# Optimization experiments

Measured on AMD Instinct MI355X. Metric: run time of the kernel, lower is better.

Reference implementation:

```python
import jax, jax.numpy as jnp
import numpy as np

N_PARENTS = 4096   # parent clusters
K = 32             # points decoded per cluster
NEIGH = 128        # neigh_dec_size
FEAT = 256         # input_size (per-parent feature dim passed through)


def setup_inputs() -> dict:
    key = jax.random.key(0)
    ks = jax.random.split(key, 6)
    def lin(k, fan_in, fan_out):
        return jax.random.normal(k, (fan_in, fan_out), jnp.float32) / np.sqrt(fan_in).astype(np.float32)
    return {
        "input_features": jax.random.normal(ks[0], (N_PARENTS, NEIGH + FEAT), jnp.float32),
        # neighborhood decoder: Linear NEIGH -> K*3 (relative points)
        "W_dec": lin(ks[1], NEIGH, K * 3), "b_dec": jnp.zeros((K * 3,), jnp.float32),
        # fc chain: (FEAT+3) -> 512 -> 512 -> 256
        "W1": lin(ks[2], FEAT + 3, 512), "b1": jnp.zeros((512,), jnp.float32),
        "W2": lin(ks[3], 512, 512),      "b2": jnp.zeros((512,), jnp.float32),
        "W3": lin(ks[4], 512, 256),      "b3": jnp.zeros((256,), jnp.float32),
    }


def reference(input_features, W_dec, b_dec, W1, b1, W2, b2, W3, b3):
    # split: first NEIGH dims go to the neighborhood decoder, rest are parent features
    neigh_feats = input_features[:, :NEIGH]            # [N, NEIGH]
    features = input_features[:, NEIGH:]               # [N, FEAT]

    # neighborhood_dec: decode K relative 3D points per parent + cluster assignment
    relative_points = (neigh_feats @ W_dec + b_dec).reshape(-1, 3)   # [N*K, 3]
    cluster = jnp.repeat(jnp.arange(N_PARENTS, dtype=jnp.int32), K)  # [N*K]

    # gather parent features per point, concat with relative points
    features_dup = features[cluster]                                  # [N*K, FEAT]
    h = jnp.concatenate([features_dup, relative_points], axis=1)      # [N*K, FEAT+3]

    # chained Linear + ReLU (leaky=False)
    h = jax.nn.relu(h @ W1 + b1)
    h = jax.nn.relu(h @ W2 + b2)
    h = jax.nn.relu(h @ W3 + b3)
    return relative_points, h, cluster
```

## Files before the change

kernel.cpp:

```cpp
#include <hip/hip_runtime.h>
#include <hip/hip_bf16.h>

typedef unsigned short u16;
typedef unsigned int   u32;

#define NP     4096
#define NCH    131072
#define HBASE  393216
#define CLBASE 33947648

#define WS_W2F   0
#define WS_W3F   524288
#define WS_W1AF  786432
#define WS_F1    1048576

using bf16x8 = __attribute__((ext_vector_type(8))) short;
using f32x4  = __attribute__((ext_vector_type(4))) float;

__device__ inline u16 f2bf(float x) {
  union { float f; u32 u; } v; v.f = x;
  u32 r = v.u + 0x7FFFu + ((v.u >> 16) & 1u);
  return (u16)(r >> 16);
}
__device__ inline u32 pack2(float a, float b) {
  return (u32)f2bf(a) | ((u32)f2bf(b) << 16);
}

__global__ __launch_bounds__(256) void k_prep(const float* __restrict__ W1,
                                              const float* __restrict__ W2,
                                              const float* __restrict__ W3,
                                              u16* __restrict__ w1af,
                                              u16* __restrict__ w2f,
                                              u16* __restrict__ w3f,
                                              float* __restrict__ out) {
  int b = blockIdx.x, t = threadIdx.x;
  if (b >= 512) {
    int idx = (b - 512) * 256 + t;
    out[CLBASE + idx] = (float)(idx >> 5);
    return;
  }
  __shared__ float tile[32][33];
  const float* src; u16* dst; int pitchN, kt, nt, nkc;
  if (b < 128)      { src = W1; dst = w1af; pitchN = 512; kt = b & 7;  nt = b >> 3; nkc = 8;  }
  else if (b < 384) { int bb = b - 128; src = W2; dst = w2f; pitchN = 512; kt = bb & 15; nt = bb >> 4; nkc = 16; }
  else              { int bb = b - 384; src = W3; dst = w3f; pitchN = 256; kt = bb & 15; nt = bb >> 4; nkc = 16; }
  {
    int kk = t >> 3, n4 = (t & 7) * 4;
    const float4 v = *(const float4*)(src + (kt * 32 + kk) * pitchN + nt * 32 + n4);
    tile[kk][n4 + 0] = v.x; tile[kk][n4 + 1] = v.y;
    tile[kk][n4 + 2] = v.z; tile[kk][n4 + 3] = v.w;
  }
  __syncthreads();
  {
    int s = t >> 1, half = t & 1, fr = s >> 6, l = s & 63;
    int n_l = fr * 16 + (l & 15);
    int k_l = (l >> 4) * 8 + half * 4;
    uint2 o;
    o.x = pack2(tile[k_l + 0][n_l], tile[k_l + 1][n_l]);
    o.y = pack2(tile[k_l + 2][n_l], tile[k_l + 3][n_l]);
    int frag_id = (nt * 2 + fr) * nkc + kt;
    *(uint2*)(dst + frag_id * 512 + l * 8 + half * 4) = o;
  }
}

__global__ __launch_bounds__(512) void k_rel(const float* __restrict__ in_feats,
                                             const float* __restrict__ Wd,
                                             const float* __restrict__ bd,
                                             float* __restrict__ out) {
  int p0 = blockIdx.x * 4, t = threadIdx.x;
  __shared__ float wd[12288];
  __shared__ float ne[512];
  __shared__ float bds[96];
#pragma unroll
  for (int i = 0; i < 6; ++i)
    *(float4*)(wd + (i * 512 + t) * 4) = *(const float4*)(Wd + (i * 512 + t) * 4);
  { int pp = t >> 7, k = t & 127; ne[t] = in_feats[(p0 + pp) * 384 + k]; }
  if (t < 96) bds[t] = bd[t];
  __syncthreads();
  if (t < 384) {
    int pp = t / 96, c = t - pp * 96;
    float acc = bds[c];
    const float* nep = ne + pp * 128;
#pragma unroll 4
    for (int k = 0; k < 128; ++k) acc += nep[k] * wd[k * 96 + c];
    out[(p0 + pp) * 96 + c] = acc;
  }
}

__global__ __launch_bounds__(512, 2) void k_f1(const float* __restrict__ in_feats,
                                               const float* __restrict__ b1,
                                               const u16* __restrict__ w1af,
                                               float* __restrict__ F1) {
  int p0 = blockIdx.x * 16;
  int tid = threadIdx.x, lane = tid & 63, w = tid >> 6;
  __shared__ u16 sh_a[16 * 256];
  __shared__ float b1s[512];
  b1s[tid] = b1[tid];
  {
    int r = tid >> 5, k0 = (tid & 31) * 8;
    const float4 v0 = *(const float4*)(in_feats + (p0 + r) * 384 + 128 + k0);
    const float4 v1 = *(const float4*)(in_feats + (p0 + r) * 384 + 128 + k0 + 4);
    uint4 o;
    o.x = pack2(v0.x, v0.y); o.y = pack2(v0.z, v0.w);
    o.z = pack2(v1.x, v1.y); o.w = pack2(v1.z, v1.w);
    int slot = (k0 >> 3) ^ (r & 7);
    *(uint4*)(sh_a + r * 256 + slot * 8) = o;
  }
  __syncthreads();
  f32x4 acc[4];
#pragma unroll
  for (int i = 0; i < 4; ++i) acc[i] = f32x4{0.f, 0.f, 0.f, 0.f};
  int col = lane & 15, q8 = (lane >> 4) * 8;
#pragma unroll
  for (int kc = 0; kc < 8; ++kc) {
    int slot = ((kc * 32 + q8) >> 3) ^ (col & 7);
    bf16x8 a = *(const bf16x8*)(sh_a + col * 256 + slot * 8);
#pragma unroll
    for (int nf = 0; nf < 4; ++nf) {
      bf16x8 bfr = *(const bf16x8*)(w1af + ((w * 4 + nf) * 8 + kc) * 512 + lane * 8);
      acc[nf] = __builtin_amdgcn_mfma_f32_16x16x32_bf16(a, bfr, acc[nf], 0, 0, 0);
    }
  }
  int rb = (lane >> 4) * 4;
#pragma unroll
  for (int nf = 0; nf < 4; ++nf) {
    int n = w * 64 + nf * 16 + col;
#pragma unroll
    for (int i = 0; i < 4; ++i)
      F1[(p0 + rb + i) * 512 + n] = acc[nf][i] + b1s[n];
  }
}

__global__ __launch_bounds__(512, 2) void k_main(const float* __restrict__ W1,
                                                 const float* __restrict__ b2,
                                                 const float* __restrict__ b3,
                                                 const u16* __restrict__ w2f,
                                                 const u16* __restrict__ w3f,
                                                 const float* __restrict__ F1,
                                                 float* __restrict__ out) {
  int blk = blockIdx.x;
  int tid = threadIdx.x, lane = tid & 63, w = tid >> 6;
  __shared__ u16 sh_h[128 * 512];
  __shared__ float f1s[2048], w1bs[1536], b2s[512], b3s[256], rels[384];

  *(float4*)(f1s + tid * 4) = *(const float4*)(F1 + blk * 2048 + tid * 4);
  w1bs[tid]        = W1[131072 + tid];
  w1bs[tid + 512]  = W1[131072 + 512 + tid];
  w1bs[tid + 1024] = W1[131072 + 1024 + tid];
  b2s[tid] = b2[tid];
  if (tid < 256) b3s[tid] = b3[tid];
  if (tid < 384) rels[tid] = out[blk * 384 + tid];
  __syncthreads();

  {
    int rbase = tid & 31, g = tid >> 5;
#pragma unroll
    for (int rr = 0; rr < 128; rr += 32) {
      int r = rr + rbase, pp = r >> 5;
      float r0 = rels[r * 3 + 0], r1 = rels[r * 3 + 1], r2 = rels[r * 3 + 2];
#pragma unroll
      for (int gg = 0; gg < 8; ++gg) {
        int c4 = g * 4 + gg * 64;
        const float4 f  = *(const float4*)(f1s + pp * 512 + c4);
        const float4 w0 = *(const float4*)(w1bs + c4);
        const float4 w1v = *(const float4*)(w1bs + 512 + c4);
        const float4 w2v = *(const float4*)(w1bs + 1024 + c4);
        float v0 = fmaxf(f.x + r0 * w0.x + r1 * w1v.x + r2 * w2v.x, 0.f);
        float v1 = fmaxf(f.y + r0 * w0.y + r1 * w1v.y + r2 * w2v.y, 0.f);
        float v2 = fmaxf(f.z + r0 * w0.z + r1 * w1v.z + r2 * w2v.z, 0.f);
        float v3 = fmaxf(f.w + r0 * w0.w + r1 * w1v.w + r2 * w2v.w, 0.f);
        uint2 o; o.x = pack2(v0, v1); o.y = pack2(v2, v3);
        int slot = (c4 >> 3) ^ (r & 7);
        *(uint2*)(sh_h + r * 512 + slot * 8 + (g & 1) * 4) = o;
      }
    }
  }
  __syncthreads();

  int col = lane & 15, q8 = (lane >> 4) * 8;

  f32x4 acc2[8][4];
#pragma unroll
  for (int mf = 0; mf < 8; ++mf)
#pragma unroll
    for (int nf = 0; nf < 4; ++nf) acc2[mf][nf] = f32x4{0.f, 0.f, 0.f, 0.f};
#pragma unroll 2
  for (int kc = 0; kc < 16; ++kc) {
    bf16x8 bfr[4];
#pragma unroll
    for (int nf = 0; nf < 4; ++nf)
      bfr[nf] = *(const bf16x8*)(w2f + ((w * 4 + nf) * 16 + kc) * 512 + lane * 8);
#pragma unroll
    for (int mf = 0; mf < 8; ++mf) {
      int row = mf * 16 + col;
      int slot = ((kc * 32 + q8) >> 3) ^ (row & 7);
      bf16x8 a = *(const bf16x8*)(sh_h + row * 512 + slot * 8);
#pragma unroll
      for (int nf = 0; nf < 4; ++nf)
        acc2[mf][nf] = __builtin_amdgcn_mfma_f32_16x16x32_bf16(a, bfr[nf], acc2[mf][nf], 0, 0, 0);
    }
  }
  __syncthreads();

  {
    int rq = (lane >> 4) * 4;
#pragma unroll
    for (int mf = 0; mf < 8; ++mf)
#pragma unroll
      for (int nf = 0; nf < 4; ++nf) {
        int n = w * 64 + nf * 16 + col;
#pragma unroll
        for (int i = 0; i < 4; ++i) {
          int r = mf * 16 + rq + i;
          float v = fmaxf(acc2[mf][nf][i] + b2s[n], 0.f);
          sh_h[r * 512 + (((n >> 3) ^ (r & 7)) << 3) + (n & 7)] = f2bf(v);
        }
      }
  }
  __syncthreads();

  f32x4 acc3[8][2];
#pragma unroll
  for (int mf = 0; mf < 8; ++mf)
#pragma unroll
    for (int nf = 0; nf < 2; ++nf) acc3[mf][nf] = f32x4{0.f, 0.f, 0.f, 0.f};
#pragma unroll 2
  for (int kc = 0; kc < 16; ++kc) {
    bf16x8 bfr[2];
#pragma unroll
    for (int nf = 0; nf < 2; ++nf)
      bfr[nf] = *(const bf16x8*)(w3f + ((w * 2 + nf) * 16 + kc) * 512 + lane * 8);
#pragma unroll
    for (int mf = 0; mf < 8; ++mf) {
      int row = mf * 16 + col;
      int slot = ((kc * 32 + q8) >> 3) ^ (row & 7);
      bf16x8 a = *(const bf16x8*)(sh_h + row * 512 + slot * 8);
#pragma unroll
      for (int nf = 0; nf < 2; ++nf)
        acc3[mf][nf] = __builtin_amdgcn_mfma_f32_16x16x32_bf16(a, bfr[nf], acc3[mf][nf], 0, 0, 0);
    }
  }

  {
    int rq = (lane >> 4) * 4;
#pragma unroll
    for (int mf = 0; mf < 8; ++mf)
#pragma unroll
      for (int nf = 0; nf < 2; ++nf) {
        int n = w * 32 + nf * 16 + col;
#pragma unroll
        for (int i = 0; i < 4; ++i) {
          int r = mf * 16 + rq + i;
          float v = fmaxf(acc3[mf][nf][i] + b3s[n], 0.f);
          out[HBASE + (blk * 128 + r) * 256 + n] = v;
        }
      }
  }
}

extern "C" void kernel_launch(void* const* d_in, const int* in_sizes, int n_in,
                              void* d_out, int out_size, void* d_ws, size_t ws_size,
                              hipStream_t stream) {
  const float* in_feats = (const float*)d_in[0];
  const float* Wd = (const float*)d_in[1];
  const float* bd = (const float*)d_in[2];
  const float* W1 = (const float*)d_in[3];
  const float* b1 = (const float*)d_in[4];
  const float* W2 = (const float*)d_in[5];
  const float* b2 = (const float*)d_in[6];
  const float* W3 = (const float*)d_in[7];
  const float* b3 = (const float*)d_in[8];
  float* out = (float*)d_out;
  char* ws = (char*)d_ws;
  u16*   w2f  = (u16*)(ws + WS_W2F);
  u16*   w3f  = (u16*)(ws + WS_W3F);
  u16*   w1af = (u16*)(ws + WS_W1AF);
  float* F1   = (float*)(ws + WS_F1);

  k_prep<<<1024, 256, 0, stream>>>(W1, W2, W3, w1af, w2f, w3f, out);
  k_rel<<<1024, 512, 0, stream>>>(in_feats, Wd, bd, out);
  k_f1<<<256, 512, 0, stream>>>(in_feats, b1, w1af, F1);
  k_main<<<1024, 512, 0, stream>>>(W1, b2, b3, w2f, w3f, F1, out);
}
```

Baseline: 272.6 us.

## Merge prep kernels into one launch and double-buffer weight fragments in main GEMMs

Folds the weight-prep, relative-point decoder, first-layer feature GEMM and cluster-index fill into a single multi-role kernel, dropping three launches to one. W1 is now read directly from fp32 and packed to bf16 inside the F1 GEMM instead of through a pre-swizzled buffer. In the main kernel the W2/W3 B-fragments are double-buffered across k-steps, the LDS swizzle gains extra row bits, the layer-1 build writes 16-byte chunks, and outputs use nontemporal stores. Risks include uncoalesced strided W1 reads in the F1 path and higher register pressure from double buffering.

```diff
diff --git a/kernel.cpp b/kernel.cpp
--- a/kernel.cpp
+++ b/kernel.cpp
@@ -11,123 +11,128 @@
 
 #define WS_W2F   0
 #define WS_W3F   524288
-#define WS_W1AF  786432
 #define WS_F1    1048576
 
 using bf16x8 = __attribute__((ext_vector_type(8))) short;
 using f32x4  = __attribute__((ext_vector_type(4))) float;
 
-__device__ inline u16 f2bf(float x) {
-  union { float f; u32 u; } v; v.f = x;
-  u32 r = v.u + 0x7FFFu + ((v.u >> 16) & 1u);
-  return (u16)(r >> 16);
-}
-__device__ inline u32 pack2(float a, float b) {
-  return (u32)f2bf(a) | ((u32)f2bf(b) << 16);
-}
-
-__global__ __launch_bounds__(256) void k_prep(const float* __restrict__ W1,
-                                              const float* __restrict__ W2,
-                                              const float* __restrict__ W3,
-                                              u16* __restrict__ w1af,
-                                              u16* __restrict__ w2f,
-                                              u16* __restrict__ w3f,
-                                              float* __restrict__ out) {
-  int b = blockIdx.x, t = threadIdx.x;
-  if (b >= 512) {
-    int idx = (b - 512) * 256 + t;
-    out[CLBASE + idx] = (float)(idx >> 5);
-    return;
-  }
-  __shared__ float tile[32][33];
-  const float* src; u16* dst; int pitchN, kt, nt, nkc;
-  if (b < 128)      { src = W1; dst = w1af; pitchN = 512; kt = b & 7;  nt = b >> 3; nkc = 8;  }
-  else if (b < 384) { int bb = b - 128; src = W2; dst = w2f; pitchN = 512; kt = bb & 15; nt = bb >> 4; nkc = 16; }
-  else              { int bb = b - 384; src = W3; dst = w3f; pitchN = 256; kt = bb & 15; nt = bb >> 4; nkc = 16; }
-  {
-    int kk = t >> 3, n4 = (t & 7) * 4;
-    const float4 v = *(const float4*)(src + (kt * 32 + kk) * pitchN + nt * 32 + n4);
-    tile[kk][n4 + 0] = v.x; tile[kk][n4 + 1] = v.y;
-    tile[kk][n4 + 2] = v.z; tile[kk][n4 + 3] = v.w;
-  }
-  __syncthreads();
-  {
-    int s = t >> 1, half = t & 1, fr = s >> 6, l = s & 63;
-    int n_l = fr * 16 + (l & 15);
-    int k_l = (l >> 4) * 8 + half * 4;
-    uint2 o;
-    o.x = pack2(tile[k_l + 0][n_l], tile[k_l + 1][n_l]);
-    o.y = pack2(tile[k_l + 2][n_l], tile[k_l + 3][n_l]);
-    int frag_id = (nt * 2 + fr) * nkc + kt;
-    *(uint2*)(dst + frag_id * 512 + l * 8 + half * 4) = o;
-  }
-}
-
-__global__ __launch_bounds__(512) void k_rel(const float* __restrict__ in_feats,
-                                             const float* __restrict__ Wd,
-                                             const float* __restrict__ bd,
-                                             float* __restrict__ out) {
-  int p0 = blockIdx.x * 4, t = threadIdx.x;
-  __shared__ float wd[12288];
-  __shared__ float ne[512];
-  __shared__ float bds[96];
-#pragma unroll
-  for (int i = 0; i < 6; ++i)
-    *(float4*)(wd + (i * 512 + t) * 4) = *(const float4*)(Wd + (i * 512 + t) * 4);
-  { int pp = t >> 7, k = t & 127; ne[t] = in_feats[(p0 + pp) * 384 + k]; }
-  if (t < 96) bds[t] = bd[t];
-  __syncthreads();
-  if (t < 384) {
-    int pp = t / 96, c = t - pp * 96;
-    float acc = bds[c];
-    const float* nep = ne + pp * 128;
+__device__ inline u32 pk2(float a, float b) {
+  __hip_bfloat162 h = __float22bfloat162_rn(make_float2(a, b));
+  return *reinterpret_cast<u32*>(&h);
+}
+
+__device__ inline int swz(int r, int cg) {
+  return cg ^ (r & 7) ^ ((r >> 3) & 3);
+}
+
+__global__ __launch_bounds__(512, 2) void k_pre(const float* __restrict__ in_feats,
+                                                const float* __restrict__ Wd,
+                                                const float* __restrict__ bd,
+                                                const float* __restrict__ W1,
+                                                const float* __restrict__ b1,
+                                                const float* __restrict__ W2,
+                                                const float* __restrict__ W3,
+                                                u16* __restrict__ w2f,
+                                                u16* __restrict__ w3f,
+                                                float* __restrict__ F1,
+                                                float* __restrict__ out) {
+  __shared__ __align__(16) char smem[51584];
+  int b = blockIdx.x, tid = threadIdx.x;
+
+  if (b < 256) {
+    u16*   sh_a = (u16*)smem;
+    float* b1s  = (float*)(smem + 8192);
+    int p0 = b * 16, lane = tid & 63, w = tid >> 6;
+    b1s[tid] = b1[tid];
+    {
+      int r = tid >> 5, k0 = (tid & 31) * 8;
+      const float4 v0 = *(const float4*)(in_feats + (p0 + r) * 384 + 128 + k0);
+      const float4 v1 = *(const float4*)(in_feats + (p0 + r) * 384 + 128 + k0 + 4);
+      uint4 o;
+      o.x = pk2(v0.x, v0.y); o.y = pk2(v0.z, v0.w);
+      o.z = pk2(v1.x, v1.y); o.w = pk2(v1.z, v1.w);
+      int slot = (k0 >> 3) ^ (r & 7);
+      *(uint4*)(sh_a + r * 256 + slot * 8) = o;
+    }
+    __syncthreads();
+    f32x4 acc[4];
+#pragma unroll
+    for (int i = 0; i < 4; ++i) acc[i] = f32x4{0.f, 0.f, 0.f, 0.f};
+    int col = lane & 15, q = lane >> 4, q8 = q * 8;
+#pragma unroll
+    for (int kc = 0; kc < 8; ++kc) {
+      int slot = ((kc * 32 + q8) >> 3) ^ (col & 7);
+      bf16x8 a = *(const bf16x8*)(sh_a + col * 256 + slot * 8);
+#pragma unroll
+      for (int nf = 0; nf < 4; ++nf) {
+        const float* wp = W1 + (kc * 32 + q8) * 512 + (w * 4 + nf) * 16 + col;
+        float v0 = wp[0],      v1 = wp[512],  v2 = wp[1024], v3 = wp[1536];
+        float v4 = wp[2048],   v5 = wp[2560], v6 = wp[3072], v7 = wp[3584];
+        union { bf16x8 v; u32 u[4]; } uu;
+        uu.u[0] = pk2(v0, v1); uu.u[1] = pk2(v2, v3);
+        uu.u[2] = pk2(v4, v5); uu.u[3] = pk2(v6, v7);
+        acc[nf] = __builtin_amdgcn_mfma_f32_16x16x32_bf16(a, uu.v, acc[nf], 0, 0, 0);
+      }
+    }
+    int rb = (lane >> 4) * 4;
+#pragma unroll
+    for (int nf = 0; nf < 4; ++nf) {
+      int n = w * 64 + nf * 16 + col;
+#pragma unroll
+      for (int i = 0; i < 4; ++i)
+        F1[(p0 + rb + i) * 512 + n] = acc[nf][i] + b1s[n];
+    }
+  } else if (b < 1280) {
+    float* wd  = (float*)smem;
+    float* ne  = (float*)(smem + 49152);
+    float* bds = (float*)(smem + 51200);
+    int p0 = (b - 256) * 4, t = tid;
+#pragma unroll
+    for (int i = 0; i < 6; ++i)
+      *(float4*)(wd + (i * 512 + t) * 4) = *(const float4*)(Wd + (i * 512 + t) * 4);
+    { int pp = t >> 7, k = t & 127; ne[t] = in_feats[(p0 + pp) * 384 + k]; }
+    if (t < 96) bds[t] = bd[t];
+    __syncthreads();
+    if (t < 384) {
+      int pp = t / 96, c = t - pp * 96;
+      float acc = bds[c];
+      const float* nep = ne + pp * 128;
 #pragma unroll 4
-    for (int k = 0; k < 128; ++k) acc += nep[k] * wd[k * 96 + c];
-    out[(p0 + pp) * 96 + c] = acc;
-  }
-}
-
-__global__ __launch_bounds__(512, 2) void k_f1(const float* __restrict__ in_feats,
-                                               const float* __restrict__ b1,
-                                               const u16* __restrict__ w1af,
-                                               float* __restrict__ F1) {
-  int p0 = blockIdx.x * 16;
-  int tid = threadIdx.x, lane = tid & 63, w = tid >> 6;
-  __shared__ u16 sh_a[16 * 256];
-  __shared__ float b1s[512];
-  b1s[tid] = b1[tid];
-  {
-    int r = tid >> 5, k0 = (tid & 31) * 8;
-    const float4 v0 = *(const float4*)(in_feats + (p0 + r) * 384 + 128 + k0);
-    const float4 v1 = *(const float4*)(in_feats + (p0 + r) * 384 + 128 + k0 + 4);
-    uint4 o;
-    o.x = pack2(v0.x, v0.y); o.y = pack2(v0.z, v0.w);
-    o.z = pack2(v1.x, v1.y); o.w = pack2(v1.z, v1.w);
-    int slot = (k0 >> 3) ^ (r & 7);
-    *(uint4*)(sh_a + r * 256 + slot * 8) = o;
-  }
-  __syncthreads();
-  f32x4 acc[4];
-#pragma unroll
-  for (int i = 0; i < 4; ++i) acc[i] = f32x4{0.f, 0.f, 0.f, 0.f};
-  int col = lane & 15, q8 = (lane >> 4) * 8;
-#pragma unroll
-  for (int kc = 0; kc < 8; ++kc) {
-    int slot = ((kc * 32 + q8) >> 3) ^ (col & 7);
-    bf16x8 a = *(const bf16x8*)(sh_a + col * 256 + slot * 8);
-#pragma unroll
-    for (int nf = 0; nf < 4; ++nf) {
-      bf16x8 bfr = *(const bf16x8*)(w1af + ((w * 4 + nf) * 8 + kc) * 512 + lane * 8);
-      acc[nf] = __builtin_amdgcn_mfma_f32_16x16x32_bf16(a, bfr, acc[nf], 0, 0, 0);
-    }
-  }
-  int rb = (lane >> 4) * 4;
-#pragma unroll
-  for (int nf = 0; nf < 4; ++nf) {
-    int n = w * 64 + nf * 16 + col;
-#pragma unroll
-    for (int i = 0; i < 4; ++i)
-      F1[(p0 + rb + i) * 512 + n] = acc[nf][i] + b1s[n];
+      for (int k = 0; k < 128; ++k) acc += nep[k] * wd[k * 96 + c];
+      out[(p0 + pp) * 96 + c] = acc;
+    }
+  } else if (b < 1472) {
+    float (*tile)[32][33] = (float (*)[32][33])smem;
+    int h = tid >> 8, t = tid & 255;
+    const float* src; u16* dst; int pitchN, g;
+    if (b < 1408) { g = (b - 1280) * 2 + h; src = W2; dst = w2f; pitchN = 512; }
+    else          { g = (b - 1408) * 2 + h; src = W3; dst = w3f; pitchN = 256; }
+    int kt = g & 15, nt = g >> 4;
+    {
+      int kk = t >> 3, n4 = (t & 7) * 4;
+      const float4 v = *(const float4*)(src + (kt * 32 + kk) * pitchN + nt * 32 + n4);
+      tile[h][kk][n4 + 0] = v.x; tile[h][kk][n4 + 1] = v.y;
+      tile[h][kk][n4 + 2] = v.z; tile[h][kk][n4 + 3] = v.w;
+    }
+    __syncthreads();
+    {
+      int s = t >> 1, half = t & 1, fr = s >> 6, l = s & 63;
+      int n_l = fr * 16 + (l & 15);
+      int k_l = (l >> 4) * 8 + half * 4;
+      uint2 o;
+      o.x = pk2(tile[h][k_l + 0][n_l], tile[h][k_l + 1][n_l]);
+      o.y = pk2(tile[h][k_l + 2][n_l], tile[h][k_l + 3][n_l]);
+      int frag_id = (nt * 2 + fr) * 16 + kt;
+      *(uint2*)(dst + frag_id * 512 + l * 8 + half * 4) = o;
+    }
+  } else {
+    int idx = ((b - 1472) * 512 + tid) * 4;
+    float c = (float)(idx >> 5);
+    float* p = out + CLBASE + idx;
+    __builtin_nontemporal_store(c, p + 0);
+    __builtin_nontemporal_store(c, p + 1);
+    __builtin_nontemporal_store(c, p + 2);
+    __builtin_nontemporal_store(c, p + 3);
   }
 }
 
@@ -153,25 +158,34 @@
   __syncthreads();
 
   {
-    int rbase = tid & 31, g = tid >> 5;
+    int r = tid & 31, g = tid >> 5;
 #pragma unroll
     for (int rr = 0; rr < 128; rr += 32) {
-      int r = rr + rbase, pp = r >> 5;
-      float r0 = rels[r * 3 + 0], r1 = rels[r * 3 + 1], r2 = rels[r * 3 + 2];
-#pragma unroll
-      for (int gg = 0; gg < 8; ++gg) {
-        int c4 = g * 4 + gg * 64;
-        const float4 f  = *(const float4*)(f1s + pp * 512 + c4);
-        const float4 w0 = *(const float4*)(w1bs + c4);
-        const float4 w1v = *(const float4*)(w1bs + 512 + c4);
-        const float4 w2v = *(const float4*)(w1bs + 1024 + c4);
-        float v0 = fmaxf(f.x + r0 * w0.x + r1 * w1v.x + r2 * w2v.x, 0.f);
-        float v1 = fmaxf(f.y + r0 * w0.y + r1 * w1v.y + r2 * w2v.y, 0.f);
-        float v2 = fmaxf(f.z + r0 * w0.z + r1 * w1v.z + r2 * w2v.z, 0.f);
-        float v3 = fmaxf(f.w + r0 * w0.w + r1 * w1v.w + r2 * w2v.w, 0.f);
-        uint2 o; o.x = pack2(v0, v1); o.y = pack2(v2, v3);
-        int slot = (c4 >> 3) ^ (r & 7);
-        *(uint2*)(sh_h + r * 512 + slot * 8 + (g & 1) * 4) = o;
+      int row = rr + r, pp = rr >> 5;
+      float r0 = rels[row * 3 + 0], r1 = rels[row * 3 + 1], r2 = rels[row * 3 + 2];
+#pragma unroll
+      for (int gg = 0; gg < 4; ++gg) {
+        int c8 = g * 8 + gg * 128;
+        const float4 fa = *(const float4*)(f1s + pp * 512 + c8);
+        const float4 fb = *(const float4*)(f1s + pp * 512 + c8 + 4);
+        const float4 wa0 = *(const float4*)(w1bs + c8);
+        const float4 wb0 = *(const float4*)(w1bs + c8 + 4);
+        const float4 wa1 = *(const float4*)(w1bs + 512 + c8);
+        const float4 wb1 = *(const float4*)(w1bs + 512 + c8 + 4);
+        const float4 wa2 = *(const float4*)(w1bs + 1024 + c8);
+        const float4 wb2 = *(const float4*)(w1bs + 1024 + c8 + 4);
+        float v0 = fmaxf(fa.x + r0 * wa0.x + r1 * wa1.x + r2 * wa2.x, 0.f);
+        float v1 = fmaxf(fa.y + r0 * wa0.y + r1 * wa1.y + r2 * wa2.y, 0.f);
+        float v2 = fmaxf(fa.z + r0 * wa0.z + r1 * wa1.z + r2 * wa2.z, 0.f);
+        float v3 = fmaxf(fa.w + r0 * wa0.w + r1 * wa1.w + r2 * wa2.w, 0.f);
+        float v4 = fmaxf(fb.x + r0 * wb0.x + r1 * wb1.x + r2 * wb2.x, 0.f);
+        float v5 = fmaxf(fb.y + r0 * wb0.y + r1 * wb1.y + r2 * wb2.y, 0.f);
+        float v6 = fmaxf(fb.z + r0 * wb0.z + r1 * wb1.z + r2 * wb2.z, 0.f);
+        float v7 = fmaxf(fb.w + r0 * wb0.w + r1 * wb1.w + r2 * wb2.w, 0.f);
+        uint4 o;
+        o.x = pk2(v0, v1); o.y = pk2(v2, v3);
+        o.z = pk2(v4, v5); o.w = pk2(v6, v7);
+        *(uint4*)(sh_h + row * 512 + swz(row, c8 >> 3) * 8) = o;
       }
     }
   }
@@ -184,20 +198,29 @@
   for (int mf = 0; mf < 8; ++mf)
 #pragma unroll
     for (int nf = 0; nf < 4; ++nf) acc2[mf][nf] = f32x4{0.f, 0.f, 0.f, 0.f};
+  {
+    const u16* w2p = w2f + (size_t)(w * 4 * 16) * 512 + lane * 8;
+    bf16x8 bufA[4], bufB[4];
+#pragma unroll
+    for (int nf = 0; nf < 4; ++nf) bufA[nf] = *(const bf16x8*)(w2p + nf * 16 * 512);
 #pragma unroll 2
-  for (int kc = 0; kc < 16; ++kc) {
-    bf16x8 bfr[4];
-#pragma unroll
-    for (int nf = 0; nf < 4; ++nf)
-      bfr[nf] = *(const bf16x8*)(w2f + ((w * 4 + nf) * 16 + kc) * 512 + lane * 8);
-#pragma unroll
-    for (int mf = 0; mf < 8; ++mf) {
-      int row = mf * 16 + col;
-      int slot = ((kc * 32 + q8) >> 3) ^ (row & 7);
-      bf16x8 a = *(const bf16x8*)(sh_h + row * 512 + slot * 8);
-#pragma unroll
-      for (int nf = 0; nf < 4; ++nf)
-        acc2[mf][nf] = __builtin_amdgcn_mfma_f32_16x16x32_bf16(a, bfr[nf], acc2[mf][nf], 0, 0, 0);
+    for (int kc = 0; kc < 16; ++kc) {
+      const bf16x8* cur = (kc & 1) ? bufB : bufA;
+      bf16x8* nxt = (kc & 1) ? bufA : bufB;
+      if (kc < 15) {
+#pragma unroll
+        for (int nf = 0; nf < 4; ++nf)
+          nxt[nf] = *(const bf16x8*)(w2p + (nf * 16 + kc + 1) * 512);
+      }
+      int cb = (kc * 32 + q8) >> 3;
+#pragma unroll
+      for (int mf = 0; mf < 8; ++mf) {
+        int row = mf * 16 + col;
+        bf16x8 a = *(const bf16x8*)(sh_h + row * 512 + swz(row, cb) * 8);
+#pragma unroll
+        for (int nf = 0; nf < 4; ++nf)
+          acc2[mf][nf] = __builtin_amdgcn_mfma_f32_16x16x32_bf16(a, cur[nf], acc2[mf][nf], 0, 0, 0);
+      }
     }
   }
   __syncthreads();
@@ -208,51 +231,64 @@
     for (int mf = 0; mf < 8; ++mf)
 #pragma unroll
       for (int nf = 0; nf < 4; ++nf) {
-        int n = w * 64 + nf * 16 + col;
+        int n = w * 64 + nf * 16 + col, cg = n >> 3, n7 = n & 7;
+        float bv = b2s[n];
+#pragma unroll
+        for (int i = 0; i < 4; i += 2) {
+          int r0 = mf * 16 + rq + i, r1 = r0 + 1;
+          u32 p = pk2(fmaxf(acc2[mf][nf][i] + bv, 0.f),
+                      fmaxf(acc2[mf][nf][i + 1] + bv, 0.f));
+          sh_h[r0 * 512 + swz(r0, cg) * 8 + n7] = (u16)(p & 0xffff);
+          sh_h[r1 * 512 + swz(r1, cg) * 8 + n7] = (u16)(p >> 16);
+        }
+      }
+  }
+  __syncthreads();
+
+  f32x4 acc3[8][2];
+#pragma unroll
+  for (int mf = 0; mf < 8; ++mf)
+#pragma unroll
+    for (int nf = 0; nf < 2; ++nf) acc3[mf][nf] = f32x4{0.f, 0.f, 0.f, 0.f};
+  {
+    const u16* w3p = w3f + (size_t)(w * 2 * 16) * 512 + lane * 8;
+    bf16x8 bufA[2], bufB[2];
+#pragma unroll
+    for (int nf = 0; nf < 2; ++nf) bufA[nf] = *(const bf16x8*)(w3p + nf * 16 * 512);
+#pragma unroll 2
+    for (int kc = 0; kc < 16; ++kc) {
+      const bf16x8* cur = (kc & 1) ? bufB : bufA;
+      bf16x8* nxt = (kc & 1) ? bufA : bufB;
+      if (kc < 15) {
+#pragma unroll
+        for (int nf = 0; nf < 2; ++nf)
+          nxt[nf] = *(const bf16x8*)(w3p + (nf * 16 + kc + 1) * 512);
+      }
+      int cb = (kc * 32 + q8) >> 3;
+#pragma unroll
+      for (int mf = 0; mf < 8; ++mf) {
+        int row = mf * 16 + col;
+        bf16x8 a = *(const bf16x8*)(sh_h + row * 512 + swz(row, cb) * 8);
+#pragma unroll
+        for (int nf = 0; nf < 2; ++nf)
+          acc3[mf][nf] = __builtin_amdgcn_mfma_f32_16x16x32_bf16(a, cur[nf], acc3[mf][nf], 0, 0, 0);
+      }
+    }
+  }
+
+  {
+    int rq = (lane >> 4) * 4;
+#pragma unroll
+    for (int mf = 0; mf < 8; ++mf)
+#pragma unroll
+      for (int nf = 0; nf < 2; ++nf) {
+        int n = w * 32 + nf * 16 + col;
+        float bv = b3s[n];
 #pragma unroll
         for (int i = 0; i < 4; ++i) {
           int r = mf * 16 + rq + i;
-          float v = fmaxf(acc2[mf][nf][i] + b2s[n], 0.f);
-          sh_h[r * 512 + (((n >> 3) ^ (r & 7)) << 3) + (n & 7)] = f2bf(v);
-        }
-      }
-  }
-  __syncthreads();
-
-  f32x4 acc3[8][2];
-#pragma unroll
-  for (int mf = 0; mf < 8; ++mf)
-#pragma unroll
-    for (int nf = 0; nf < 2; ++nf) acc3[mf][nf] = f32x4{0.f, 0.f, 0.f, 0.f};
-#pragma unroll 2
-  for (int kc = 0; kc < 16; ++kc) {
-    bf16x8 bfr[2];
-#pragma unroll
-    for (int nf = 0; nf < 2; ++nf)
-      bfr[nf] = *(const bf16x8*)(w3f + ((w * 2 + nf) * 16 + kc) * 512 + lane * 8);
-#pragma unroll
-    for (int mf = 0; mf < 8; ++mf) {
-      int row = mf * 16 + col;
-      int slot = ((kc * 32 + q8) >> 3) ^ (row & 7);
-      bf16x8 a = *(const bf16x8*)(sh_h + row * 512 + slot * 8);
-#pragma unroll
-      for (int nf = 0; nf < 2; ++nf)
-        acc3[mf][nf] = __builtin_amdgcn_mfma_f32_16x16x32_bf16(a, bfr[nf], acc3[mf][nf], 0, 0, 0);
-    }
-  }
-
-  {
-    int rq = (lane >> 4) * 4;
-#pragma unroll
-    for (int mf = 0; mf < 8; ++mf)
-#pragma unroll
-      for (int nf = 0; nf < 2; ++nf) {
-        int n = w * 32 + nf * 16 + col;
-#pragma unroll
-        for (int i = 0; i < 4; ++i) {
-          int r = mf * 16 + rq + i;
-          float v = fmaxf(acc3[mf][nf][i] + b3s[n], 0.f);
-          out[HBASE + (blk * 128 + r) * 256 + n] = v;
+          float v = fmaxf(acc3[mf][nf][i] + bv, 0.f);
+          __builtin_nontemporal_store(v, out + HBASE + (blk * 128 + r) * 256 + n);
         }
       }
   }
@@ -272,13 +308,10 @@
   const float* b3 = (const float*)d_in[8];
   float* out = (float*)d_out;
   char* ws = (char*)d_ws;
-  u16*   w2f  = (u16*)(ws + WS_W2F);
-  u16*   w3f  = (u16*)(ws + WS_W3F);
-  u16*   w1af = (u16*)(ws + WS_W1AF);
-  float* F1   = (float*)(ws + WS_F1);
-
-  k_prep<<<1024, 256, 0, stream>>>(W1, W2, W3, w1af, w2f, w3f, out);
-  k_rel<<<1024, 512, 0, stream>>>(in_feats, Wd, bd, out);
-  k_f1<<<256, 512, 0, stream>>>(in_feats, b1, w1af, F1);
+  u16*   w2f = (u16*)(ws + WS_W2F);
+  u16*   w3f = (u16*)(ws + WS_W3F);
+  float* F1  = (float*)(ws + WS_F1);
+
+  k_pre<<<1536, 512, 0, stream>>>(in_feats, Wd, bd, W1, b1, W2, W3, w2f, w3f, F1, out);
   k_main<<<1024, 512, 0, stream>>>(W1, b2, b3, w2f, w3f, F1, out);
 }
```

New measurement: 276.2 us. Within noise of the previous version (+1.3%).
